# Kernel optimization log

Hardware: AMD Instinct MI355X
Metric: run time of the kernel (lower is better)

The kernel has to match this reference:

```python
import jax, jax.numpy as jnp
import numpy as np

HIDDEN = 64
CLASSES = 5


def setup_inputs() -> dict:
    key = jax.random.key(0)
    ks = jax.random.split(key, 7)
    B, T = 512, 3600
    s = 1.0 / np.sqrt(HIDDEN)  # PyTorch GRU init scale
    x = jax.random.normal(ks[0], (B, T, 1), dtype=jnp.float32)
    w_ih = jax.random.uniform(ks[1], (3 * HIDDEN, 1), jnp.float32, -s, s)
    w_hh = jax.random.uniform(ks[2], (3 * HIDDEN, HIDDEN), jnp.float32, -s, s)
    b_ih = jax.random.uniform(ks[3], (3 * HIDDEN,), jnp.float32, -s, s)
    b_hh = jax.random.uniform(ks[4], (3 * HIDDEN,), jnp.float32, -s, s)
    w_head = jax.random.uniform(ks[5], (CLASSES, HIDDEN), jnp.float32, -s, s)
    b_head = jax.random.uniform(ks[6], (CLASSES,), jnp.float32, -s, s)
    return {"x": x, "w_ih": w_ih, "w_hh": w_hh, "b_ih": b_ih,
            "b_hh": b_hh, "w_head": w_head, "b_head": b_head}


def reference(x, w_ih, w_hh, b_ih, b_hh, w_head, b_head):
    # x: [B, T, 1]; single-layer GRU (PyTorch gate ordering r, z, n), h0 = 0.
    B, T, _ = x.shape
    H = w_hh.shape[1]
    # Precompute input projections for all timesteps: [T, B, 3H]
    gi = jnp.einsum('bti,gi->tbg', x, w_ih) + b_ih

    def step(h, gi_t):
        gh = h @ w_hh.T + b_hh                      # [B, 3H]
        i_r, i_z, i_n = jnp.split(gi_t, 3, axis=-1)
        h_r, h_z, h_n = jnp.split(gh, 3, axis=-1)
        r = jax.nn.sigmoid(i_r + h_r)
        z = jax.nn.sigmoid(i_z + h_z)
        n = jnp.tanh(i_n + r * h_n)
        h_new = (1.0 - z) * n + z * h
        return h_new, None

    h0 = jnp.zeros((B, H), dtype=x.dtype)
    h_last, _ = jax.lax.scan(step, h0, gi)
    # head on last hidden state: [B, classes]
    return h_last @ w_head.T + b_head
```

## Files before the change

kernel.cpp:

```cpp
#include <hip/hip_runtime.h>
#include <math.h>

#define BATCH   512
#define TSTEPS  3600
#define H       64
#define XCHUNK  16
#define NCHUNK  (TSTEPS / XCHUNK)
#define CLASSES 5

typedef _Float16 half8 __attribute__((ext_vector_type(8)));
typedef float    f32x4 __attribute__((ext_vector_type(4)));

__device__ __forceinline__ half8 bc_h8(uint4 v) {
    return __builtin_bit_cast(half8, v);
}

#define L2E 1.44269504088896f
#define S_N (2.0f * L2E)

__global__ __launch_bounds__(256, 1) void gru_mfma_kernel(
    const float* __restrict__ x,
    const float* __restrict__ w_ih,
    const float* __restrict__ w_hh,
    const float* __restrict__ b_ih,
    const float* __restrict__ b_hh,
    const float* __restrict__ w_head,
    const float* __restrict__ b_head,
    float* __restrict__ out)
{
    __shared__ __align__(16) _Float16 hl[2][H];
    __shared__ float hf[H];

    const int tid  = threadIdx.x;
    const int w    = tid >> 6;
    const int lane = tid & 63;
    const int q    = lane >> 4;
    const int col  = lane & 15;
    const int b    = blockIdx.x;
    const int i    = 16 * w + col;

    half8 wR[2], wZ[2], wN[2];
#pragma unroll
    for (int c = 0; c < 2; ++c) {
        const float* pr = w_hh + (16 * w       + col) * H + 32 * c + 8 * q;
        const float* pz = w_hh + (16 * (4 + w) + col) * H + 32 * c + 8 * q;
        const float* pn = w_hh + (16 * (8 + w) + col) * H + 32 * c + 8 * q;
        half8 fr, fz, fn;
#pragma unroll
        for (int j = 0; j < 8; ++j) {
            fr[j] = (_Float16)(-L2E * pr[j]);
            fz[j] = (_Float16)(-L2E * pz[j]);
            fn[j] = (_Float16)( S_N * pn[j]);
        }
        wR[c] = fr; wZ[c] = fz; wN[c] = fn;
    }

    const float bn = S_N * b_hh[2 * H + i];
    const f32x4 Cn = {bn, bn, bn, bn};
    const f32x4 Z  = {0.f, 0.f, 0.f, 0.f};

    const float wih_r = -L2E * w_ih[i];
    const float wih_z = -L2E * w_ih[H + i];
    const float wih_n =  S_N * w_ih[2 * H + i];
    const float bsr = -L2E * (b_ih[i] + b_hh[i]);
    const float bsz = -L2E * (b_ih[H + i] + b_hh[H + i]);
    const float bin =  S_N * b_ih[2 * H + i];

    float h_reg = 0.0f;
    if (lane < 16) hl[0][16 * w + lane] = (_Float16)0.0f;
    __syncthreads();

    const float* xb = x + (size_t)b * TSTEPS;
    float vxc = xb[col];

    for (int tc = 0; tc < NCHUNK; ++tc) {
        const float* nxt = xb + ((tc + 1 < NCHUNK) ? (tc + 1) * XCHUNK : 0);
        const float vxn = nxt[col];

#pragma unroll
        for (int tt = 0; tt < XCHUNK; ++tt) {
            const uint4* hp = (const uint4*)hl[tt & 1];
            const half8 A0 = bc_h8(hp[q]);
            const half8 A1 = bc_h8(hp[4 + q]);

            const float xt = __builtin_bit_cast(float,
                __builtin_amdgcn_readlane(__builtin_bit_cast(int, vxc), tt));
            const float ir  = fmaf(xt, wih_r, bsr);
            const float iz  = fmaf(xt, wih_z, bsz);
            const float in_ = fmaf(xt, wih_n, bin);

            f32x4 dr, dz, dn;
            dr = __builtin_amdgcn_mfma_f32_16x16x32_f16(A0, wR[0], Z,  0, 0, 0);
            dz = __builtin_amdgcn_mfma_f32_16x16x32_f16(A0, wZ[0], Z,  0, 0, 0);
            dn = __builtin_amdgcn_mfma_f32_16x16x32_f16(A0, wN[0], Cn, 0, 0, 0);
            dr = __builtin_amdgcn_mfma_f32_16x16x32_f16(A1, wR[1], dr, 0, 0, 0);
            dz = __builtin_amdgcn_mfma_f32_16x16x32_f16(A1, wZ[1], dz, 0, 0, 0);
            dn = __builtin_amdgcn_mfma_f32_16x16x32_f16(A1, wN[1], dn, 0, 0, 0);

            const float er = __builtin_amdgcn_exp2f(ir + dr[0]);
            const float r  = __builtin_amdgcn_rcpf(1.0f + er);
            const float ez = __builtin_amdgcn_exp2f(iz + dz[0]);
            const float z  = __builtin_amdgcn_rcpf(1.0f + ez);
            const float ev = __builtin_amdgcn_exp2f(fmaf(r, dn[0], in_));
            const float nn = (ev - 1.0f) * __builtin_amdgcn_rcpf(ev + 1.0f);
            h_reg = fmaf(z, h_reg - nn, nn);

            if (lane < 16) hl[(tt & 1) ^ 1][16 * w + lane] = (_Float16)h_reg;
            __syncthreads();
        }
        vxc = vxn;
    }

    if (lane < 16) hf[16 * w + lane] = h_reg;
    __syncthreads();
    if (w == 0) {
        const float hv = hf[lane];
#pragma unroll
        for (int cc = 0; cc < CLASSES; ++cc) {
            float v = hv * w_head[cc * H + lane];
#pragma unroll
            for (int off = 32; off > 0; off >>= 1)
                v += __shfl_down(v, off, 64);
            if (lane == 0) out[b * CLASSES + cc] = v + b_head[cc];
        }
    }
}

extern "C" void kernel_launch(void* const* d_in, const int* in_sizes, int n_in,
                              void* d_out, int out_size, void* d_ws, size_t ws_size,
                              hipStream_t stream) {
    const float* x      = (const float*)d_in[0];
    const float* w_ih   = (const float*)d_in[1];
    const float* w_hh   = (const float*)d_in[2];
    const float* b_ih   = (const float*)d_in[3];
    const float* b_hh   = (const float*)d_in[4];
    const float* w_head = (const float*)d_in[5];
    const float* b_head = (const float*)d_in[6];
    float* out = (float*)d_out;

    gru_mfma_kernel<<<BATCH, 256, 0, stream>>>(x, w_ih, w_hh, b_ih, b_hh,
                                               w_head, b_head, out);
}
```

Baseline: 803.6 us.

## Interleave four batch rows per block and split MFMA dependency chains

Each block now advances four independent batch sequences in lockstep, so MFMA, transcendental and LDS latency of one sequence can overlap with the others, and one barrier per step serves four rows. The grid shrinks from 512 to 128 blocks. The K-halves of each gate are issued as independent MFMAs that are summed afterwards. Input projections are folded into the accumulator init and computed one step ahead. The risk is that only half the CUs are used and each step carries four rows' worth of serial work.

```diff
diff --git a/kernel.cpp b/kernel.cpp
--- a/kernel.cpp
+++ b/kernel.cpp
@@ -1,22 +1,21 @@
 #include <hip/hip_runtime.h>
-#include <math.h>
 
 #define BATCH   512
+#define G       4
+#define NBLK    (BATCH / G)
 #define TSTEPS  3600
 #define H       64
-#define XCHUNK  16
+#define XCHUNK  8
 #define NCHUNK  (TSTEPS / XCHUNK)
 #define CLASSES 5
 
 typedef _Float16 half8 __attribute__((ext_vector_type(8)));
 typedef float    f32x4 __attribute__((ext_vector_type(4)));
 
-__device__ __forceinline__ half8 bc_h8(uint4 v) {
-    return __builtin_bit_cast(half8, v);
-}
-
 #define L2E 1.44269504088896f
 #define S_N (2.0f * L2E)
+
+__device__ __forceinline__ half8 bc_h8(uint4 v) { return __builtin_bit_cast(half8, v); }
 
 __global__ __launch_bounds__(256, 1) void gru_mfma_kernel(
     const float* __restrict__ x,
@@ -28,7 +27,7 @@
     const float* __restrict__ b_head,
     float* __restrict__ out)
 {
-    __shared__ __align__(16) _Float16 hl[2][H];
+    __shared__ __align__(16) _Float16 hbuf[G * 2 * 4 * 80];
     __shared__ float hf[H];
 
     const int tid  = threadIdx.x;
@@ -36,7 +35,7 @@
     const int lane = tid & 63;
     const int q    = lane >> 4;
     const int col  = lane & 15;
-    const int b    = blockIdx.x;
+    const int b0   = blockIdx.x * G;
     const int i    = 16 * w + col;
 
     half8 wR[2], wZ[2], wN[2];
@@ -66,63 +65,115 @@
     const float bsz = -L2E * (b_ih[H + i] + b_hh[H + i]);
     const float bin =  S_N * b_ih[2 * H + i];
 
-    float h_reg = 0.0f;
-    if (lane < 16) hl[0][16 * w + lane] = (_Float16)0.0f;
+    char* hb = (char*)hbuf;
+    const int woff  = q * 160 + i * 2;
+    const int roff0 = 176 * q;
+    const int roff1 = 176 * q + 64;
+
+#pragma unroll
+    for (int g = 0; g < G; ++g)
+        *(_Float16*)(hb + g * 1280 + woff) = (_Float16)0.0f;
     __syncthreads();
 
-    const float* xb = x + (size_t)b * TSTEPS;
-    float vxc = xb[col];
+    float hreg[G], hm1[G], irc[G], izc[G], inc[G], vxc[G], vxn[G];
+#pragma unroll
+    for (int g = 0; g < G; ++g) {
+        hreg[g] = 0.0f; hm1[g] = -1.0f;
+        vxc[g] = x[(size_t)(b0 + g) * TSTEPS + (col & 7)];
+        const float xt0 = __builtin_bit_cast(float,
+            __builtin_amdgcn_readlane(__builtin_bit_cast(int, vxc[g]), 0));
+        irc[g] = fmaf(xt0, wih_r, bsr);
+        izc[g] = fmaf(xt0, wih_z, bsz);
+        inc[g] = fmaf(xt0, wih_n, bin);
+    }
 
     for (int tc = 0; tc < NCHUNK; ++tc) {
-        const float* nxt = xb + ((tc + 1 < NCHUNK) ? (tc + 1) * XCHUNK : 0);
-        const float vxn = nxt[col];
+        const int nb = (tc + 1 < NCHUNK) ? (tc + 1) * XCHUNK : 0;
+#pragma unroll
+        for (int g = 0; g < G; ++g)
+            vxn[g] = x[(size_t)(b0 + g) * TSTEPS + nb + (col & 7)];
 
 #pragma unroll
         for (int tt = 0; tt < XCHUNK; ++tt) {
-            const uint4* hp = (const uint4*)hl[tt & 1];
-            const half8 A0 = bc_h8(hp[q]);
-            const half8 A1 = bc_h8(hp[4 + q]);
+            const int pr = (tt & 1) * 640;
+            const int pw = ((tt & 1) ^ 1) * 640;
 
-            const float xt = __builtin_bit_cast(float,
-                __builtin_amdgcn_readlane(__builtin_bit_cast(int, vxc), tt));
-            const float ir  = fmaf(xt, wih_r, bsr);
-            const float iz  = fmaf(xt, wih_z, bsz);
-            const float in_ = fmaf(xt, wih_n, bin);
+            uint4 a0u[G], a1u[G];
+#pragma unroll
+            for (int g = 0; g < G; ++g) {
+                a0u[g] = *(const uint4*)(hb + g * 1280 + pr + roff0);
+                a1u[g] = *(const uint4*)(hb + g * 1280 + pr + roff1);
+            }
 
-            f32x4 dr, dz, dn;
-            dr = __builtin_amdgcn_mfma_f32_16x16x32_f16(A0, wR[0], Z,  0, 0, 0);
-            dz = __builtin_amdgcn_mfma_f32_16x16x32_f16(A0, wZ[0], Z,  0, 0, 0);
-            dn = __builtin_amdgcn_mfma_f32_16x16x32_f16(A0, wN[0], Cn, 0, 0, 0);
-            dr = __builtin_amdgcn_mfma_f32_16x16x32_f16(A1, wR[1], dr, 0, 0, 0);
-            dz = __builtin_amdgcn_mfma_f32_16x16x32_f16(A1, wZ[1], dz, 0, 0, 0);
-            dn = __builtin_amdgcn_mfma_f32_16x16x32_f16(A1, wN[1], dn, 0, 0, 0);
+            f32x4 r0[G], r1[G], n0[G], n1[G], z0[G], z1[G];
+#pragma unroll
+            for (int g = 0; g < G; ++g) {
+                const half8 A0 = bc_h8(a0u[g]);
+                const half8 A1 = bc_h8(a1u[g]);
+                const f32x4 Cr = {irc[g], irc[g], irc[g], irc[g]};
+                const f32x4 Cz = {izc[g], izc[g], izc[g], izc[g]};
+                r0[g] = __builtin_amdgcn_mfma_f32_16x16x32_f16(A0, wR[0], Cr, 0, 0, 0);
+                r1[g] = __builtin_amdgcn_mfma_f32_16x16x32_f16(A1, wR[1], Z,  0, 0, 0);
+                n0[g] = __builtin_amdgcn_mfma_f32_16x16x32_f16(A0, wN[0], Cn, 0, 0, 0);
+                n1[g] = __builtin_amdgcn_mfma_f32_16x16x32_f16(A1, wN[1], Z,  0, 0, 0);
+                z0[g] = __builtin_amdgcn_mfma_f32_16x16x32_f16(A0, wZ[0], Cz, 0, 0, 0);
+                z1[g] = __builtin_amdgcn_mfma_f32_16x16x32_f16(A1, wZ[1], Z,  0, 0, 0);
+            }
 
-            const float er = __builtin_amdgcn_exp2f(ir + dr[0]);
-            const float r  = __builtin_amdgcn_rcpf(1.0f + er);
-            const float ez = __builtin_amdgcn_exp2f(iz + dz[0]);
-            const float z  = __builtin_amdgcn_rcpf(1.0f + ez);
-            const float ev = __builtin_amdgcn_exp2f(fmaf(r, dn[0], in_));
-            const float nn = (ev - 1.0f) * __builtin_amdgcn_rcpf(ev + 1.0f);
-            h_reg = fmaf(z, h_reg - nn, nn);
+            float irn[G], izn[G], inn[G];
+#pragma unroll
+            for (int g = 0; g < G; ++g) {
+                const float vxs = (tt == XCHUNK - 1) ? vxn[g] : vxc[g];
+                const float xtn = __builtin_bit_cast(float,
+                    __builtin_amdgcn_readlane(__builtin_bit_cast(int, vxs),
+                                              (tt + 1) & (XCHUNK - 1)));
+                irn[g] = fmaf(xtn, wih_r, bsr);
+                izn[g] = fmaf(xtn, wih_z, bsz);
+                inn[g] = fmaf(xtn, wih_n, bin);
+            }
 
-            if (lane < 16) hl[(tt & 1) ^ 1][16 * w + lane] = (_Float16)h_reg;
+#pragma unroll
+            for (int g = 0; g < G; ++g) {
+                const float er = __builtin_amdgcn_exp2f(r0[g][0] + r1[g][0]);
+                const float rg = __builtin_amdgcn_rcpf(1.0f + er);
+                const float ev = __builtin_amdgcn_exp2f(
+                                     fmaf(rg, n0[g][0] + n1[g][0], inc[g]));
+                const float u  = __builtin_amdgcn_rcpf(ev + 1.0f);
+                const float nn = fmaf(-2.0f, u, 1.0f);
+                const float s  = fmaf(2.0f, u, hm1[g]);
+                const float ez = __builtin_amdgcn_exp2f(z0[g][0] + z1[g][0]);
+                const float zg = __builtin_amdgcn_rcpf(1.0f + ez);
+                hreg[g] = fmaf(zg, s, nn);
+                hm1[g]  = hreg[g] - 1.0f;
+                *(_Float16*)(hb + g * 1280 + pw + woff) = (_Float16)hreg[g];
+            }
             __syncthreads();
+
+#pragma unroll
+            for (int g = 0; g < G; ++g) {
+                irc[g] = irn[g]; izc[g] = izn[g]; inc[g] = inn[g];
+            }
         }
-        vxc = vxn;
+#pragma unroll
+        for (int g = 0; g < G; ++g) vxc[g] = vxn[g];
     }
 
-    if (lane < 16) hf[16 * w + lane] = h_reg;
-    __syncthreads();
-    if (w == 0) {
-        const float hv = hf[lane];
 #pragma unroll
-        for (int cc = 0; cc < CLASSES; ++cc) {
-            float v = hv * w_head[cc * H + lane];
+    for (int g = 0; g < G; ++g) {
+        if (lane < 16) hf[i] = hreg[g];
+        __syncthreads();
+        if (w == 0) {
+            const float hv = hf[lane];
 #pragma unroll
-            for (int off = 32; off > 0; off >>= 1)
-                v += __shfl_down(v, off, 64);
-            if (lane == 0) out[b * CLASSES + cc] = v + b_head[cc];
+            for (int cc = 0; cc < CLASSES; ++cc) {
+                float v = hv * w_head[cc * H + lane];
+#pragma unroll
+                for (int off = 32; off > 0; off >>= 1)
+                    v += __shfl_down(v, off, 64);
+                if (lane == 0) out[(b0 + g) * CLASSES + cc] = v + b_head[cc];
+            }
         }
+        __syncthreads();
     }
 }
 
@@ -138,6 +189,6 @@
     const float* b_head = (const float*)d_in[6];
     float* out = (float*)d_out;
 
-    gru_mfma_kernel<<<BATCH, 256, 0, stream>>>(x, w_ih, w_hh, b_ih, b_hh,
-                                               w_head, b_head, out);
+    gru_mfma_kernel<<<NBLK, 256, 0, stream>>>(x, w_ih, w_hh, b_ih, b_hh,
+                                              w_head, b_head, out);
 }
```

After: 2.156 ms. 168% more time.

## Process four batch rows per block using spare MFMA rows

Applied to the files above, without the earlier changes.

Each block now handles 4 batch elements, filling 4 of the 16 MFMA A-matrix rows instead of 1, so the grid shrinks from 512 to 128 blocks. Each lane group q handles its own batch row and writes its hidden state into a padded shared buffer. Input projections are folded into the MFMA accumulators and prefetched one step ahead via ds_bpermute. The tanh/update math is also reformulated to save ops. With only 128 blocks on a 256-CU device, per-block sequential latency dominates, and each step now does more work per lane.

```diff
diff --git a/kernel.cpp b/kernel.cpp
--- a/kernel.cpp
+++ b/kernel.cpp
@@ -1,7 +1,8 @@
 #include <hip/hip_runtime.h>
-#include <math.h>
 
 #define BATCH   512
+#define GB      4
+#define NBLK    (BATCH / GB)
 #define TSTEPS  3600
 #define H       64
 #define XCHUNK  16
@@ -11,12 +12,10 @@
 typedef _Float16 half8 __attribute__((ext_vector_type(8)));
 typedef float    f32x4 __attribute__((ext_vector_type(4)));
 
-__device__ __forceinline__ half8 bc_h8(uint4 v) {
-    return __builtin_bit_cast(half8, v);
-}
-
 #define L2E 1.44269504088896f
 #define S_N (2.0f * L2E)
+
+__device__ __forceinline__ half8 bc_h8(uint4 v) { return __builtin_bit_cast(half8, v); }
 
 __global__ __launch_bounds__(256, 1) void gru_mfma_kernel(
     const float* __restrict__ x,
@@ -28,15 +27,15 @@
     const float* __restrict__ b_head,
     float* __restrict__ out)
 {
-    __shared__ __align__(16) _Float16 hl[2][H];
-    __shared__ float hf[H];
+    __shared__ __align__(16) _Float16 hB[2][GB * 80];
+    __shared__ float hf[GB][H];
 
     const int tid  = threadIdx.x;
     const int w    = tid >> 6;
     const int lane = tid & 63;
     const int q    = lane >> 4;
     const int col  = lane & 15;
-    const int b    = blockIdx.x;
+    const int b0   = blockIdx.x * GB;
     const int i    = 16 * w + col;
 
     half8 wR[2], wZ[2], wN[2];
@@ -56,8 +55,9 @@
     }
 
     const float bn = S_N * b_hh[2 * H + i];
-    const f32x4 Cn = {bn, bn, bn, bn};
-    const f32x4 Z  = {0.f, 0.f, 0.f, 0.f};
+    f32x4 Cn = {bn, bn, bn, bn};
+    const f32x4 Z = {0.f, 0.f, 0.f, 0.f};
+    f32x4 Cr = Z, Cz = Z;
 
     const float wih_r = -L2E * w_ih[i];
     const float wih_z = -L2E * w_ih[H + i];
@@ -66,62 +66,88 @@
     const float bsz = -L2E * (b_ih[H + i] + b_hh[H + i]);
     const float bin =  S_N * b_ih[2 * H + i];
 
-    float h_reg = 0.0f;
-    if (lane < 16) hl[0][16 * w + lane] = (_Float16)0.0f;
+    char* hbase = (char*)&hB[0][0];
+    const int rdA0 = (col >> 2) * 160 + q * 16;
+    const int rdA1 = rdA0 + 64;
+    const int wrH  = q * 160 + i * 2;
+
+    *(_Float16*)(hbase + wrH) = (_Float16)0.0f;
     __syncthreads();
 
-    const float* xb = x + (size_t)b * TSTEPS;
-    float vxc = xb[col];
+    const float* xq = x + (size_t)(b0 + q) * TSTEPS;
+    float vx = xq[col];
+    const int pbase = 64 * q;
+
+    float xt0 = __builtin_bit_cast(float,
+        __builtin_amdgcn_ds_bpermute(pbase, __builtin_bit_cast(int, vx)));
+    float irc = fmaf(xt0, wih_r, bsr);
+    float izc = fmaf(xt0, wih_z, bsz);
+    float inc = fmaf(xt0, wih_n, bin);
+
+    float h_reg = 0.0f, hm1 = -1.0f;
 
     for (int tc = 0; tc < NCHUNK; ++tc) {
-        const float* nxt = xb + ((tc + 1 < NCHUNK) ? (tc + 1) * XCHUNK : 0);
-        const float vxn = nxt[col];
+        const int nb = (tc + 1 < NCHUNK) ? (tc + 1) * XCHUNK : 0;
+        const float vxn = xq[nb + col];
 
 #pragma unroll
         for (int tt = 0; tt < XCHUNK; ++tt) {
-            const uint4* hp = (const uint4*)hl[tt & 1];
-            const half8 A0 = bc_h8(hp[q]);
-            const half8 A1 = bc_h8(hp[4 + q]);
+            const int pr_ = (tt & 1) * 640;
+            const int pw_ = ((tt & 1) ^ 1) * 640;
 
-            const float xt = __builtin_bit_cast(float,
-                __builtin_amdgcn_readlane(__builtin_bit_cast(int, vxc), tt));
-            const float ir  = fmaf(xt, wih_r, bsr);
-            const float iz  = fmaf(xt, wih_z, bsz);
-            const float in_ = fmaf(xt, wih_n, bin);
+            const uint4 a0 = *(const uint4*)(hbase + pr_ + rdA0);
+            const uint4 a1 = *(const uint4*)(hbase + pr_ + rdA1);
 
-            f32x4 dr, dz, dn;
-            dr = __builtin_amdgcn_mfma_f32_16x16x32_f16(A0, wR[0], Z,  0, 0, 0);
-            dz = __builtin_amdgcn_mfma_f32_16x16x32_f16(A0, wZ[0], Z,  0, 0, 0);
+            const float xsrc = (tt == XCHUNK - 1) ? vxn : vx;
+            const float xtn = __builtin_bit_cast(float,
+                __builtin_amdgcn_ds_bpermute(pbase + 4 * ((tt + 1) & 15),
+                                             __builtin_bit_cast(int, xsrc)));
+
+            Cr[0] = irc;
+            Cz[0] = izc;
+
+            const half8 A0 = bc_h8(a0);
+            const half8 A1 = bc_h8(a1);
+            f32x4 dr, dn, dz;
+            dr = __builtin_amdgcn_mfma_f32_16x16x32_f16(A0, wR[0], Cr, 0, 0, 0);
+            dr = __builtin_amdgcn_mfma_f32_16x16x32_f16(A1, wR[1], dr, 0, 0, 0);
             dn = __builtin_amdgcn_mfma_f32_16x16x32_f16(A0, wN[0], Cn, 0, 0, 0);
-            dr = __builtin_amdgcn_mfma_f32_16x16x32_f16(A1, wR[1], dr, 0, 0, 0);
+            dn = __builtin_amdgcn_mfma_f32_16x16x32_f16(A1, wN[1], dn, 0, 0, 0);
+            dz = __builtin_amdgcn_mfma_f32_16x16x32_f16(A0, wZ[0], Cz, 0, 0, 0);
             dz = __builtin_amdgcn_mfma_f32_16x16x32_f16(A1, wZ[1], dz, 0, 0, 0);
-            dn = __builtin_amdgcn_mfma_f32_16x16x32_f16(A1, wN[1], dn, 0, 0, 0);
 
-            const float er = __builtin_amdgcn_exp2f(ir + dr[0]);
+            const float er = __builtin_amdgcn_exp2f(dr[0]);
             const float r  = __builtin_amdgcn_rcpf(1.0f + er);
-            const float ez = __builtin_amdgcn_exp2f(iz + dz[0]);
-            const float z  = __builtin_amdgcn_rcpf(1.0f + ez);
-            const float ev = __builtin_amdgcn_exp2f(fmaf(r, dn[0], in_));
-            const float nn = (ev - 1.0f) * __builtin_amdgcn_rcpf(ev + 1.0f);
-            h_reg = fmaf(z, h_reg - nn, nn);
+            const float ev = __builtin_amdgcn_exp2f(fmaf(r, dn[0], inc));
+            const float u  = __builtin_amdgcn_rcpf(ev + 1.0f);
+            const float nn = fmaf(-2.0f, u, 1.0f);
+            const float s  = fmaf(2.0f, u, hm1);
+            const float ez = __builtin_amdgcn_exp2f(dz[0]);
+            const float zg = __builtin_amdgcn_rcpf(1.0f + ez);
+            h_reg = fmaf(zg, s, nn);
+            hm1   = h_reg - 1.0f;
 
-            if (lane < 16) hl[(tt & 1) ^ 1][16 * w + lane] = (_Float16)h_reg;
+            irc = fmaf(xtn, wih_r, bsr);
+            izc = fmaf(xtn, wih_z, bsz);
+            inc = fmaf(xtn, wih_n, bin);
+
+            *(_Float16*)(hbase + pw_ + wrH) = (_Float16)h_reg;
             __syncthreads();
         }
-        vxc = vxn;
+        vx = vxn;
     }
 
-    if (lane < 16) hf[16 * w + lane] = h_reg;
+    hf[q][i] = h_reg;
     __syncthreads();
-    if (w == 0) {
-        const float hv = hf[lane];
+    {
+        const float hv = hf[w][lane];
 #pragma unroll
         for (int cc = 0; cc < CLASSES; ++cc) {
             float v = hv * w_head[cc * H + lane];
 #pragma unroll
             for (int off = 32; off > 0; off >>= 1)
                 v += __shfl_down(v, off, 64);
-            if (lane == 0) out[b * CLASSES + cc] = v + b_head[cc];
+            if (lane == 0) out[(b0 + w) * CLASSES + cc] = v + b_head[cc];
         }
     }
 }
@@ -138,6 +164,6 @@
     const float* b_head = (const float*)d_in[6];
     float* out = (float*)d_out;
 
-    gru_mfma_kernel<<<BATCH, 256, 0, stream>>>(x, w_ih, w_hh, b_ih, b_hh,
-                                               w_head, b_head, out);
+    gru_mfma_kernel<<<NBLK, 256, 0, stream>>>(x, w_ih, w_hh, b_ih, b_hh,
+                                              w_head, b_head, out);
 }
```

New measurement: 721.1 us (median of 2 runs). -10.3%, faster.

## Pack 8 batch rows per block in two interleaved MFMA groups

Applied to the files above, without the earlier changes.

Each block now processes 8 batch rows instead of one. They form two groups of 4 rows, and each group uses 4 of the MFMA's 16 M-rows. The two groups' recurrences are interleaved so that one group's MFMA and transcendental latency can hide behind the other's, and the launch uses 64 blocks instead of 512. The input projection is folded into the MFMA accumulator, the tanh is rewritten algebraically, and the __syncthreads is replaced by a raw barrier with an explicit lgkmcnt wait. With only 64 blocks, most of the device's CUs sit idle, so total throughput depends on whether per-step latency drops enough to make up for the lower parallelism.

```diff
diff --git a/kernel.cpp b/kernel.cpp
--- a/kernel.cpp
+++ b/kernel.cpp
@@ -1,22 +1,22 @@
 #include <hip/hip_runtime.h>
-#include <math.h>
 
 #define BATCH   512
+#define GB      4
+#define GRP     2
+#define NBLK    (BATCH / (GB * GRP))
 #define TSTEPS  3600
+#define XCHUNK  8
+#define NCHUNK  (TSTEPS / XCHUNK)
 #define H       64
-#define XCHUNK  16
-#define NCHUNK  (TSTEPS / XCHUNK)
 #define CLASSES 5
 
 typedef _Float16 half8 __attribute__((ext_vector_type(8)));
 typedef float    f32x4 __attribute__((ext_vector_type(4)));
 
-__device__ __forceinline__ half8 bc_h8(uint4 v) {
-    return __builtin_bit_cast(half8, v);
-}
-
 #define L2E 1.44269504088896f
 #define S_N (2.0f * L2E)
+
+__device__ __forceinline__ half8 bc_h8(uint4 v) { return __builtin_bit_cast(half8, v); }
 
 __global__ __launch_bounds__(256, 1) void gru_mfma_kernel(
     const float* __restrict__ x,
@@ -28,15 +28,15 @@
     const float* __restrict__ b_head,
     float* __restrict__ out)
 {
-    __shared__ __align__(16) _Float16 hl[2][H];
-    __shared__ float hf[H];
+    __shared__ __align__(16) _Float16 hB[GRP][2][GB * 80];
+    __shared__ float hf[GRP * GB][H];
 
     const int tid  = threadIdx.x;
     const int w    = tid >> 6;
     const int lane = tid & 63;
     const int q    = lane >> 4;
     const int col  = lane & 15;
-    const int b    = blockIdx.x;
+    const int b0   = blockIdx.x * (GB * GRP);
     const int i    = 16 * w + col;
 
     half8 wR[2], wZ[2], wN[2];
@@ -58,6 +58,7 @@
     const float bn = S_N * b_hh[2 * H + i];
     const f32x4 Cn = {bn, bn, bn, bn};
     const f32x4 Z  = {0.f, 0.f, 0.f, 0.f};
+    f32x4 Cr0 = Z, Cz0 = Z, Cr1 = Z, Cz1 = Z;
 
     const float wih_r = -L2E * w_ih[i];
     const float wih_z = -L2E * w_ih[H + i];
@@ -66,62 +67,96 @@
     const float bsz = -L2E * (b_ih[H + i] + b_hh[H + i]);
     const float bin =  S_N * b_ih[2 * H + i];
 
-    float h_reg = 0.0f;
-    if (lane < 16) hl[0][16 * w + lane] = (_Float16)0.0f;
+    char* hb0 = (char*)&hB[0][0][0];
+    char* hb1 = (char*)&hB[1][0][0];
+    const int rdA0 = (col >> 2) * 160 + q * 16;
+    const int rdA1 = rdA0 + 64;
+    const int wrH  = q * 160 + i * 2;
+
+    *(_Float16*)(hb0 + wrH) = (_Float16)0.0f;
+    *(_Float16*)(hb1 + wrH) = (_Float16)0.0f;
     __syncthreads();
 
-    const float* xb = x + (size_t)b * TSTEPS;
-    float vxc = xb[col];
+    const float* xq0 = x + (size_t)(b0 + q)      * TSTEPS;
+    const float* xq1 = x + (size_t)(b0 + GB + q) * TSTEPS;
+    f32x4 c00 = *(const f32x4*)(xq0), c01 = *(const f32x4*)(xq0 + 4);
+    f32x4 c10 = *(const f32x4*)(xq1), c11 = *(const f32x4*)(xq1 + 4);
+
+    float h0 = 0.0f, hm10 = -1.0f, h1 = 0.0f, hm11 = -1.0f;
+
+    uint4 a00 = *(const uint4*)(hb0 + rdA0);
+    uint4 a01 = *(const uint4*)(hb0 + rdA1);
+    uint4 a10 = *(const uint4*)(hb1 + rdA0);
+    uint4 a11 = *(const uint4*)(hb1 + rdA1);
+
+#define PHASE(hb, aA, aB, CrV, CzV, hreg, hm1, XT, PW) {                       \
+    const float xt_ = (XT);                                                    \
+    CrV[0] = fmaf(xt_, wih_r, bsr);                                            \
+    CzV[0] = fmaf(xt_, wih_z, bsz);                                            \
+    const float inc_ = fmaf(xt_, wih_n, bin);                                  \
+    const half8 A0_ = bc_h8(aA), A1_ = bc_h8(aB);                              \
+    f32x4 dr_ = __builtin_amdgcn_mfma_f32_16x16x32_f16(A0_, wR[0], CrV, 0,0,0);\
+    dr_ = __builtin_amdgcn_mfma_f32_16x16x32_f16(A1_, wR[1], dr_, 0,0,0);      \
+    f32x4 dn_ = __builtin_amdgcn_mfma_f32_16x16x32_f16(A0_, wN[0], Cn, 0,0,0); \
+    dn_ = __builtin_amdgcn_mfma_f32_16x16x32_f16(A1_, wN[1], dn_, 0,0,0);      \
+    f32x4 dz_ = __builtin_amdgcn_mfma_f32_16x16x32_f16(A0_, wZ[0], CzV, 0,0,0);\
+    dz_ = __builtin_amdgcn_mfma_f32_16x16x32_f16(A1_, wZ[1], dz_, 0,0,0);      \
+    const float er_ = __builtin_amdgcn_exp2f(dr_[0]);                          \
+    const float rr_ = __builtin_amdgcn_rcpf(1.0f + er_);                       \
+    const float ev_ = __builtin_amdgcn_exp2f(fmaf(rr_, dn_[0], inc_));         \
+    const float uu_ = __builtin_amdgcn_rcpf(ev_ + 1.0f);                       \
+    const float nn_ = fmaf(-2.0f, uu_, 1.0f);                        \
+    const float ss_ = fmaf(2.0f, uu_, hm1);                        \
+    const float ez_ = __builtin_amdgcn_exp2f(dz_[0]);                          \
+    const float zg_ = __builtin_amdgcn_rcpf(1.0f + ez_);                       \
+    hreg = fmaf(zg_, ss_, nn_);                               \
+    hm1  = hreg - 1.0f;                                                        \
+    *(_Float16*)((hb) + (PW) + wrH) = (_Float16)hreg;                          \
+    asm volatile("s_waitcnt lgkmcnt(0)" ::: "memory");                         \
+    __builtin_amdgcn_s_barrier();                                              \
+    asm volatile("" ::: "memory");                                             \
+    aA = *(const uint4*)((hb) + (PW) + rdA0);          \
+    aB = *(const uint4*)((hb) + (PW) + rdA1);                                  \
+}
+
+#define STEP2(tt, X0, X1)                                                      \
+    PHASE(hb0, a00, a01, Cr0, Cz0, h0, hm10, X0, ((((tt) & 1) ^ 1) * 640))     \
+    PHASE(hb1, a10, a11, Cr1, Cz1, h1, hm11, X1, ((((tt) & 1) ^ 1) * 640))
 
     for (int tc = 0; tc < NCHUNK; ++tc) {
-        const float* nxt = xb + ((tc + 1 < NCHUNK) ? (tc + 1) * XCHUNK : 0);
-        const float vxn = nxt[col];
+        const int nb = (tc + 1 < NCHUNK) ? (tc + 1) * XCHUNK : 0;
+        const f32x4 n00 = *(const f32x4*)(xq0 + nb);
+        const f32x4 n01 = *(const f32x4*)(xq0 + nb + 4);
+        const f32x4 n10 = *(const f32x4*)(xq1 + nb);
+        const f32x4 n11 = *(const f32x4*)(xq1 + nb + 4);
 
+        STEP2(0, c00[0], c10[0])
+        STEP2(1, c00[1], c10[1])
+        STEP2(2, c00[2], c10[2])
+        STEP2(3, c00[3], c10[3])
+        STEP2(4, c01[0], c11[0])
+        STEP2(5, c01[1], c11[1])
+        STEP2(6, c01[2], c11[2])
+        STEP2(7, c01[3], c11[3])
+
+        c00 = n00; c01 = n01; c10 = n10; c11 = n11;
+    }
+#undef STEP2
+#undef PHASE
+
+    hf[q][i]      = h0;
+    hf[GB + q][i] = h1;
+    __syncthreads();
 #pragma unroll
-        for (int tt = 0; tt < XCHUNK; ++tt) {
-            const uint4* hp = (const uint4*)hl[tt & 1];
-            const half8 A0 = bc_h8(hp[q]);
-            const half8 A1 = bc_h8(hp[4 + q]);
-
-            const float xt = __builtin_bit_cast(float,
-                __builtin_amdgcn_readlane(__builtin_bit_cast(int, vxc), tt));
-            const float ir  = fmaf(xt, wih_r, bsr);
-            const float iz  = fmaf(xt, wih_z, bsz);
-            const float in_ = fmaf(xt, wih_n, bin);
-
-            f32x4 dr, dz, dn;
-            dr = __builtin_amdgcn_mfma_f32_16x16x32_f16(A0, wR[0], Z,  0, 0, 0);
-            dz = __builtin_amdgcn_mfma_f32_16x16x32_f16(A0, wZ[0], Z,  0, 0, 0);
-            dn = __builtin_amdgcn_mfma_f32_16x16x32_f16(A0, wN[0], Cn, 0, 0, 0);
-            dr = __builtin_amdgcn_mfma_f32_16x16x32_f16(A1, wR[1], dr, 0, 0, 0);
-            dz = __builtin_amdgcn_mfma_f32_16x16x32_f16(A1, wZ[1], dz, 0, 0, 0);
-            dn = __builtin_amdgcn_mfma_f32_16x16x32_f16(A1, wN[1], dn, 0, 0, 0);
-
-            const float er = __builtin_amdgcn_exp2f(ir + dr[0]);
-            const float r  = __builtin_amdgcn_rcpf(1.0f + er);
-            const float ez = __builtin_amdgcn_exp2f(iz + dz[0]);
-            const float z  = __builtin_amdgcn_rcpf(1.0f + ez);
-            const float ev = __builtin_amdgcn_exp2f(fmaf(r, dn[0], in_));
-            const float nn = (ev - 1.0f) * __builtin_amdgcn_rcpf(ev + 1.0f);
-            h_reg = fmaf(z, h_reg - nn, nn);
-
-            if (lane < 16) hl[(tt & 1) ^ 1][16 * w + lane] = (_Float16)h_reg;
-            __syncthreads();
-        }
-        vxc = vxn;
-    }
-
-    if (lane < 16) hf[16 * w + lane] = h_reg;
-    __syncthreads();
-    if (w == 0) {
-        const float hv = hf[lane];
+    for (int gg = 0; gg < GRP; ++gg) {
+        const float hv = hf[gg * GB + w][lane];
 #pragma unroll
         for (int cc = 0; cc < CLASSES; ++cc) {
             float v = hv * w_head[cc * H + lane];
 #pragma unroll
             for (int off = 32; off > 0; off >>= 1)
                 v += __shfl_down(v, off, 64);
-            if (lane == 0) out[b * CLASSES + cc] = v + b_head[cc];
+            if (lane == 0) out[(b0 + gg * GB + w) * CLASSES + cc] = v + b_head[cc];
         }
     }
 }
@@ -138,6 +173,6 @@
     const float* b_head = (const float*)d_in[6];
     float* out = (float*)d_out;
 
-    gru_mfma_kernel<<<BATCH, 256, 0, stream>>>(x, w_ih, w_hh, b_ih, b_hh,
-                                               w_head, b_head, out);
+    gru_mfma_kernel<<<NBLK, 256, 0, stream>>>(x, w_ih, w_hh, b_ih, b_hh,
+                                              w_head, b_head, out);
 }
```

Result: slower. 1.184 ms (+47.3%).
